# Kernel tuning notes

Hardware: AMD Instinct MI355X
Metric: run time of the kernel (lower is better)

The kernel has to match this reference:

```python
import jax, jax.numpy as jnp
import numpy as np

NUM_HEADS = 8
MAX_WS = 12


def _window_size(H, W, max_ws):
    common = [f for f in range(1, min(H, W) + 1) if H % f == 0 and W % f == 0 and f <= max_ws]
    return max(common) if common else min(H, W)


def _rel_index(ws):
    # static numpy computation, matches torch.meshgrid (ij) + offset logic
    coords = np.stack(np.meshgrid(np.arange(ws), np.arange(ws), indexing='ij')).reshape(2, -1)
    rel = coords[:, :, None] - coords[:, None, :]          # [2, ws^2, ws^2]
    rel = rel.transpose(1, 2, 0) + (ws - 1)                # [ws^2, ws^2, 2]
    return (rel[..., 0] * (2 * ws - 1) + rel[..., 1]).astype(np.int32)


def setup_inputs() -> dict:
    key = jax.random.key(0)
    ks = jax.random.split(key, 8)
    B, H, W, C = 8, 96, 96, 192
    N = H * W
    ws = _window_size(H, W, MAX_WS)  # 12
    x_seq = jax.random.normal(ks[0], (B, N, C), jnp.float32)
    noise_mask = jax.random.uniform(ks[1], (B, 1, H, W), jnp.float32)
    qkv_w = jax.random.normal(ks[2], (3 * C, C), jnp.float32) * 0.02
    qkv_b = jnp.zeros((3 * C,), jnp.float32)
    proj_w = jax.random.normal(ks[3], (C, C), jnp.float32) * 0.02
    proj_b = jnp.zeros((C,), jnp.float32)
    lpe_w = jax.random.normal(ks[4], (C, 1, 3, 3), jnp.float32) * 0.1  # depthwise OIHW
    lpe_b = jnp.zeros((C,), jnp.float32)
    lpe_scale = jnp.ones((1,), jnp.float32)
    bias_table = jax.random.normal(ks[5], ((2 * ws - 1) ** 2, NUM_HEADS), jnp.float32) * 0.02
    return {"x_seq": x_seq, "noise_mask": noise_mask, "qkv_w": qkv_w, "qkv_b": qkv_b,
            "proj_w": proj_w, "proj_b": proj_b, "lpe_w": lpe_w, "lpe_b": lpe_b,
            "lpe_scale": lpe_scale, "bias_table": bias_table}


def reference(x_seq, noise_mask, qkv_w, qkv_b, proj_w, proj_b, lpe_w, lpe_b, lpe_scale, bias_table):
    B, N, C = x_seq.shape
    H = W = int(round(N ** 0.5))
    heads = NUM_HEADS
    hd = C // heads
    ws = _window_size(H, W, MAX_WS)
    ws2 = ws * ws
    scale = hd ** (-0.5)

    x = x_seq.reshape(B, H, W, C)
    # window partition -> [nW, ws^2, C]
    win = x.reshape(B, H // ws, ws, W // ws, ws, C).transpose(0, 1, 3, 2, 4, 5).reshape(-1, ws2, C)

    qkv = win @ qkv_w.T + qkv_b                      # [nW, ws^2, 3C]
    qkv = qkv.reshape(-1, ws2, 3, heads, hd).transpose(2, 0, 3, 1, 4)  # [3, nW, h, ws^2, hd]
    q, k, v = qkv[0], qkv[1], qkv[2]

    attn = jnp.einsum('whqd,whkd->whqk', q, k) * scale   # [nW, h, ws^2, ws^2]
    idx = _rel_index(ws)                                  # static [ws^2, ws^2]
    bias = bias_table[idx.reshape(-1)].reshape(ws2, ws2, heads).transpose(2, 0, 1)
    attn = jax.nn.softmax(attn + bias[None], axis=-1)

    out = jnp.einsum('whqk,whkd->whqd', attn, v)          # [nW, h, ws^2, hd]
    out = out.transpose(0, 2, 1, 3).reshape(-1, ws2, C)
    out = out @ proj_w.T + proj_b

    # window reverse -> [B, H, W, C]
    x_attn = out.reshape(B, H // ws, W // ws, ws, ws, C).transpose(0, 1, 3, 2, 4, 5).reshape(B, H, W, C)

    # depthwise-conv LPE branch on NCHW input
    x_nchw = x.transpose(0, 3, 1, 2)
    lpe = jax.lax.conv_general_dilated(
        x_nchw, lpe_w, window_strides=(1, 1), padding='SAME',
        feature_group_count=C, dimension_numbers=('NCHW', 'OIHW', 'NCHW'))
    lpe = lpe + lpe_b[None, :, None, None]
    x_lpe = (lpe * lpe_scale[0] * noise_mask).transpose(0, 2, 3, 1)

    return (x_attn + x_lpe).reshape(B, N, C)
```

## Files before the change

### kernel.cpp

```cpp
#include <hip/hip_runtime.h>
#include <hip/hip_bf16.h>

constexpr int Bb   = 8;
constexpr int Hh   = 96;
constexpr int Ww   = 96;
constexpr int Cc   = 192;
constexpr int WS   = 12;
constexpr int WS2  = 144;
constexpr int HEADS= 8;
constexpr int HD   = 24;
constexpr int NWIN = Bb * (Hh/WS) * (Ww/WS);
constexpr int Mrows= NWIN * WS2;
constexpr int QKVN = 3 * Cc;

typedef __bf16 bf16x8 __attribute__((ext_vector_type(8)));
typedef float  f32x4  __attribute__((ext_vector_type(4)));

constexpr int LDP = 40;

__device__ __forceinline__ float us2f(unsigned short u) {
    unsigned int i = ((unsigned int)u) << 16;
    float f; __builtin_memcpy(&f, &i, 4);
    return f;
}
__device__ __forceinline__ unsigned short f2us(float f) {
    unsigned int i; __builtin_memcpy(&i, &f, 4);
    unsigned int lsb = (i >> 16) & 1u;
    i += 0x7fffu + lsb;
    return (unsigned short)(i >> 16);
}

__global__ __launch_bounds__(256) void qkv_gemm(
        const float* __restrict__ x,
        const float* __restrict__ w,
        const float* __restrict__ bias,
        unsigned short* __restrict__ qkv)
{
    __shared__ __bf16 As[128][LDP];
    __shared__ __bf16 Bs[64][LDP];

    const int tid = threadIdx.x;
    const int m0  = blockIdx.x * 128;
    const int n0  = blockIdx.y * 64;

    const int sa_row = tid >> 1;
    const int sa_ks  = (tid & 1) * 16;
    const int sb_row = tid >> 2;
    const int sb_ks  = (tid & 3) * 8;

    const int m    = m0 + sa_row;
    const int widx = m / WS2;
    const int pos  = m % WS2;
    const int b    = widx >> 6;
    const int wi   = (widx >> 3) & 7;
    const int wj   = widx & 7;
    const long xrow = ((long)((b * Hh + wi * WS + pos / WS) * Ww + wj * WS + pos % WS)) * Cc;
    const long brow = (long)(n0 + sb_row) * Cc;

    const int lane = tid & 63;
    const int wid  = tid >> 6;
    const int wm   = wid >> 1;
    const int wn   = wid & 1;
    const int frow = lane & 15;
    const int kblk = lane >> 4;

    f32x4 acc[4][2];
    #pragma unroll
    for (int i = 0; i < 4; ++i)
        #pragma unroll
        for (int j = 0; j < 2; ++j)
            acc[i][j] = f32x4{0.f, 0.f, 0.f, 0.f};

    for (int k0 = 0; k0 < Cc; k0 += 32) {
        {
            const float* g = x + xrow + k0 + sa_ks;
            float4 f0 = *reinterpret_cast<const float4*>(g);
            float4 f1 = *reinterpret_cast<const float4*>(g + 4);
            float4 f2 = *reinterpret_cast<const float4*>(g + 8);
            float4 f3 = *reinterpret_cast<const float4*>(g + 12);
            bf16x8 p0, p1;
            p0[0]=(__bf16)f0.x; p0[1]=(__bf16)f0.y; p0[2]=(__bf16)f0.z; p0[3]=(__bf16)f0.w;
            p0[4]=(__bf16)f1.x; p0[5]=(__bf16)f1.y; p0[6]=(__bf16)f1.z; p0[7]=(__bf16)f1.w;
            p1[0]=(__bf16)f2.x; p1[1]=(__bf16)f2.y; p1[2]=(__bf16)f2.z; p1[3]=(__bf16)f2.w;
            p1[4]=(__bf16)f3.x; p1[5]=(__bf16)f3.y; p1[6]=(__bf16)f3.z; p1[7]=(__bf16)f3.w;
            *reinterpret_cast<bf16x8*>(&As[sa_row][sa_ks])     = p0;
            *reinterpret_cast<bf16x8*>(&As[sa_row][sa_ks + 8]) = p1;
        }
        {
            const float* g = w + brow + k0 + sb_ks;
            float4 f0 = *reinterpret_cast<const float4*>(g);
            float4 f1 = *reinterpret_cast<const float4*>(g + 4);
            bf16x8 p0;
            p0[0]=(__bf16)f0.x; p0[1]=(__bf16)f0.y; p0[2]=(__bf16)f0.z; p0[3]=(__bf16)f0.w;
            p0[4]=(__bf16)f1.x; p0[5]=(__bf16)f1.y; p0[6]=(__bf16)f1.z; p0[7]=(__bf16)f1.w;
            *reinterpret_cast<bf16x8*>(&Bs[sb_row][sb_ks]) = p0;
        }
        __syncthreads();

        bf16x8 a0 = *reinterpret_cast<const bf16x8*>(&As[wm*64 +  0 + frow][kblk*8]);
        bf16x8 a1 = *reinterpret_cast<const bf16x8*>(&As[wm*64 + 16 + frow][kblk*8]);
        bf16x8 a2 = *reinterpret_cast<const bf16x8*>(&As[wm*64 + 32 + frow][kblk*8]);
        bf16x8 a3 = *reinterpret_cast<const bf16x8*>(&As[wm*64 + 48 + frow][kblk*8]);
        bf16x8 b0 = *reinterpret_cast<const bf16x8*>(&Bs[wn*32 +  0 + frow][kblk*8]);
        bf16x8 b1 = *reinterpret_cast<const bf16x8*>(&Bs[wn*32 + 16 + frow][kblk*8]);

        acc[0][0] = __builtin_amdgcn_mfma_f32_16x16x32_bf16(a0, b0, acc[0][0], 0, 0, 0);
        acc[0][1] = __builtin_amdgcn_mfma_f32_16x16x32_bf16(a0, b1, acc[0][1], 0, 0, 0);
        acc[1][0] = __builtin_amdgcn_mfma_f32_16x16x32_bf16(a1, b0, acc[1][0], 0, 0, 0);
        acc[1][1] = __builtin_amdgcn_mfma_f32_16x16x32_bf16(a1, b1, acc[1][1], 0, 0, 0);
        acc[2][0] = __builtin_amdgcn_mfma_f32_16x16x32_bf16(a2, b0, acc[2][0], 0, 0, 0);
        acc[2][1] = __builtin_amdgcn_mfma_f32_16x16x32_bf16(a2, b1, acc[2][1], 0, 0, 0);
        acc[3][0] = __builtin_amdgcn_mfma_f32_16x16x32_bf16(a3, b0, acc[3][0], 0, 0, 0);
        acc[3][1] = __builtin_amdgcn_mfma_f32_16x16x32_bf16(a3, b1, acc[3][1], 0, 0, 0);
        __syncthreads();
    }

    const int lrow = lane >> 4, lcol = lane & 15;
    #pragma unroll
    for (int fn = 0; fn < 2; ++fn) {
        const int c = n0 + wn*32 + fn*16 + lcol;
        const float bv = bias[c];
        #pragma unroll
        for (int fm = 0; fm < 4; ++fm) {
            const int rbase = m0 + wm*64 + fm*16 + lrow*4;
            #pragma unroll
            for (int r = 0; r < 4; ++r)
                qkv[(long)(rbase + r) * QKVN + c] = f2us(acc[fm][fn][r] + bv);
        }
    }
}

__global__ __launch_bounds__(192) void attn_kernel(
        const unsigned short* __restrict__ qkv,
        const float* __restrict__ btab,
        unsigned short* __restrict__ aout)
{
    __shared__ unsigned short Klds[WS2][40];
    __shared__ unsigned short Qlds[WS2][40];
    __shared__ unsigned short Vt[32][168];
    __shared__ unsigned short Pl[3][16][168];
    __shared__ float Bh[529];
    __shared__ unsigned short klut[WS2];
    __shared__ float l_inv[3][16];

    const int win  = blockIdx.x;
    const int head = blockIdx.y;
    const int tid  = threadIdx.x;

    const long base = (long)win * WS2 * QKVN;
    const int hoff  = head * HD;

    if (tid < WS2) {
        const uint4* qs = reinterpret_cast<const uint4*>(qkv + base + (long)tid * QKVN + hoff);
        const uint4* ks = reinterpret_cast<const uint4*>(qkv + base + (long)tid * QKVN + Cc + hoff);
        const uint4* vs = reinterpret_cast<const uint4*>(qkv + base + (long)tid * QKVN + 2*Cc + hoff);
        uint4 q0 = qs[0], q1 = qs[1], q2 = qs[2];
        uint4 k0 = ks[0], k1 = ks[1], k2 = ks[2];
        uint4 v0 = vs[0], v1 = vs[1], v2 = vs[2];
        *reinterpret_cast<uint4*>(&Qlds[tid][0])  = q0;
        *reinterpret_cast<uint4*>(&Qlds[tid][8])  = q1;
        *reinterpret_cast<uint4*>(&Qlds[tid][16]) = q2;
        *reinterpret_cast<uint4*>(&Qlds[tid][24]) = uint4{0,0,0,0};
        *reinterpret_cast<uint4*>(&Klds[tid][0])  = k0;
        *reinterpret_cast<uint4*>(&Klds[tid][8])  = k1;
        *reinterpret_cast<uint4*>(&Klds[tid][16]) = k2;
        *reinterpret_cast<uint4*>(&Klds[tid][24]) = uint4{0,0,0,0};
        unsigned short vr[24];
        __builtin_memcpy(&vr[0],  &v0, 16);
        __builtin_memcpy(&vr[8],  &v1, 16);
        __builtin_memcpy(&vr[16], &v2, 16);
        #pragma unroll
        for (int d = 0; d < HD; ++d)
            Vt[d][tid] = vr[d];
    }
    for (int e = tid; e < 8 * 160; e += 192)
        Vt[24 + e / 160][e % 160] = 0;
    for (int e = tid; e < 24 * 16; e += 192)
        Vt[e / 16][144 + (e & 15)] = 0;
    for (int e = tid; e < 529; e += 192)
        Bh[e] = btab[e * HEADS + head];
    if (tid < WS2)
        klut[tid] = (unsigned short)((tid / WS) * 23 + (tid % WS));
    __syncthreads();

    const int wv   = tid >> 6;
    const int lane = tid & 63;
    const int qcol = lane & 15;
    const int g    = lane >> 4;

    #pragma unroll
    for (int i = 0; i < 4; ++i) {
        const int e = lane + i * 64;
        Pl[wv][e >> 4][144 + (e & 15)] = 0;
    }

    const float scale = 0.2041241452319315f;

    #pragma unroll
    for (int ti = 0; ti < 3; ++ti) {
        const int qt = wv * 3 + ti;

        bf16x8 qb = *reinterpret_cast<const bf16x8*>(&Qlds[qt*16 + qcol][g*8]);
        f32x4 s[9];
        #pragma unroll
        for (int t = 0; t < 9; ++t) {
            bf16x8 ka = *reinterpret_cast<const bf16x8*>(&Klds[t*16 + qcol][g*8]);
            s[t] = __builtin_amdgcn_mfma_f32_16x16x32_bf16(ka, qb,
                     f32x4{0.f,0.f,0.f,0.f}, 0, 0, 0);
        }

        const int qpos = qt * 16 + qcol;
        const float bbase = (float)((qpos / WS + 11) * 23 + (qpos % WS + 11));
        float sv[9][4];
        float mx = -1e30f;
        #pragma unroll
        for (int t = 0; t < 9; ++t)
            #pragma unroll
            for (int r = 0; r < 4; ++r) {
                const int kv = t*16 + g*4 + r;
                const int rel = (int)bbase - (int)klut[kv];
                const float v = s[t][r] * scale + Bh[rel];
                sv[t][r] = v;
                mx = fmaxf(mx, v);
            }
        mx = fmaxf(mx, __shfl_xor(mx, 16));
        mx = fmaxf(mx, __shfl_xor(mx, 32));
        float sum = 0.f;
        #pragma unroll
        for (int t = 0; t < 9; ++t)
            #pragma unroll
            for (int r = 0; r < 4; ++r) {
                const float p = __expf(sv[t][r] - mx);
                sv[t][r] = p;
                sum += p;
            }
        sum += __shfl_xor(sum, 16);
        sum += __shfl_xor(sum, 32);
        if (g == 0)
            l_inv[wv][qcol] = 1.f / sum;

        #pragma unroll
        for (int t = 0; t < 9; ++t)
            #pragma unroll
            for (int r = 0; r < 4; ++r)
                Pl[wv][qcol][t*16 + g*4 + r] = f2us(sv[t][r]);

        f32x4 o0 = {0.f,0.f,0.f,0.f}, o1 = {0.f,0.f,0.f,0.f};
        #pragma unroll
        for (int ks = 0; ks < 5; ++ks) {
            bf16x8 pa  = *reinterpret_cast<const bf16x8*>(&Pl[wv][qcol][ks*32 + g*8]);
            bf16x8 vb0 = *reinterpret_cast<const bf16x8*>(&Vt[qcol     ][ks*32 + g*8]);
            bf16x8 vb1 = *reinterpret_cast<const bf16x8*>(&Vt[16 + qcol][ks*32 + g*8]);
            o0 = __builtin_amdgcn_mfma_f32_16x16x32_bf16(pa, vb0, o0, 0, 0, 0);
            o1 = __builtin_amdgcn_mfma_f32_16x16x32_bf16(pa, vb1, o1, 0, 0, 0);
        }

        #pragma unroll
        for (int idx = 0; idx < 4; ++idx) {
            const int qrow = qt*16 + g*4 + idx;
            const float li = l_inv[wv][g*4 + idx];
            const long ob = (long)(win * WS2 + qrow) * Cc + hoff;
            aout[ob + qcol] = f2us(o0[idx] * li);
            if (qcol < 8)
                aout[ob + 16 + qcol] = f2us(o1[idx] * li);
        }
    }
}

__global__ __launch_bounds__(256) void proj_gemm(
        const unsigned short* __restrict__ aout,
        const float* __restrict__ pw,
        const float* __restrict__ pb,
        float* __restrict__ out)
{
    __shared__ __bf16 As[128][LDP];
    __shared__ __bf16 Bs[64][LDP];

    const int tid = threadIdx.x;
    const int m0  = blockIdx.x * 128;
    const int n0  = blockIdx.y * 64;

    const int sa_row = tid >> 1;
    const int sa_ks  = (tid & 1) * 16;
    const int sb_row = tid >> 2;
    const int sb_ks  = (tid & 3) * 8;

    const long arow = (long)(m0 + sa_row) * Cc;
    const long brow = (long)(n0 + sb_row) * Cc;

    const int lane = tid & 63;
    const int wid  = tid >> 6;
    const int wm   = wid >> 1;
    const int wn   = wid & 1;
    const int frow = lane & 15;
    const int kblk = lane >> 4;

    f32x4 acc[4][2];
    #pragma unroll
    for (int i = 0; i < 4; ++i)
        #pragma unroll
        for (int j = 0; j < 2; ++j)
            acc[i][j] = f32x4{0.f, 0.f, 0.f, 0.f};

    for (int k0 = 0; k0 < Cc; k0 += 32) {
        {
            const unsigned short* g = aout + arow + k0 + sa_ks;
            uint4 v0 = *reinterpret_cast<const uint4*>(g);
            uint4 v1 = *reinterpret_cast<const uint4*>(g + 8);
            *reinterpret_cast<uint4*>(&As[sa_row][sa_ks])     = v0;
            *reinterpret_cast<uint4*>(&As[sa_row][sa_ks + 8]) = v1;
        }
        {
            const float* g = pw + brow + k0 + sb_ks;
            float4 f0 = *reinterpret_cast<const float4*>(g);
            float4 f1 = *reinterpret_cast<const float4*>(g + 4);
            bf16x8 p0;
            p0[0]=(__bf16)f0.x; p0[1]=(__bf16)f0.y; p0[2]=(__bf16)f0.z; p0[3]=(__bf16)f0.w;
            p0[4]=(__bf16)f1.x; p0[5]=(__bf16)f1.y; p0[6]=(__bf16)f1.z; p0[7]=(__bf16)f1.w;
            *reinterpret_cast<bf16x8*>(&Bs[sb_row][sb_ks]) = p0;
        }
        __syncthreads();

        bf16x8 a0 = *reinterpret_cast<const bf16x8*>(&As[wm*64 +  0 + frow][kblk*8]);
        bf16x8 a1 = *reinterpret_cast<const bf16x8*>(&As[wm*64 + 16 + frow][kblk*8]);
        bf16x8 a2 = *reinterpret_cast<const bf16x8*>(&As[wm*64 + 32 + frow][kblk*8]);
        bf16x8 a3 = *reinterpret_cast<const bf16x8*>(&As[wm*64 + 48 + frow][kblk*8]);
        bf16x8 b0 = *reinterpret_cast<const bf16x8*>(&Bs[wn*32 +  0 + frow][kblk*8]);
        bf16x8 b1 = *reinterpret_cast<const bf16x8*>(&Bs[wn*32 + 16 + frow][kblk*8]);

        acc[0][0] = __builtin_amdgcn_mfma_f32_16x16x32_bf16(a0, b0, acc[0][0], 0, 0, 0);
        acc[0][1] = __builtin_amdgcn_mfma_f32_16x16x32_bf16(a0, b1, acc[0][1], 0, 0, 0);
        acc[1][0] = __builtin_amdgcn_mfma_f32_16x16x32_bf16(a1, b0, acc[1][0], 0, 0, 0);
        acc[1][1] = __builtin_amdgcn_mfma_f32_16x16x32_bf16(a1, b1, acc[1][1], 0, 0, 0);
        acc[2][0] = __builtin_amdgcn_mfma_f32_16x16x32_bf16(a2, b0, acc[2][0], 0, 0, 0);
        acc[2][1] = __builtin_amdgcn_mfma_f32_16x16x32_bf16(a2, b1, acc[2][1], 0, 0, 0);
        acc[3][0] = __builtin_amdgcn_mfma_f32_16x16x32_bf16(a3, b0, acc[3][0], 0, 0, 0);
        acc[3][1] = __builtin_amdgcn_mfma_f32_16x16x32_bf16(a3, b1, acc[3][1], 0, 0, 0);
        __syncthreads();
    }

    const int lrow = lane >> 4, lcol = lane & 15;

    #pragma unroll
    for (int fm = 0; fm < 4; ++fm) {
        #pragma unroll
        for (int r = 0; r < 4; ++r) {
            const int mrow = m0 + wm*64 + fm*16 + lrow*4 + r;
            const int widx = mrow / WS2;
            const int pos  = mrow % WS2;
            const int b    = widx >> 6;
            const int wi   = (widx >> 3) & 7;
            const int wj   = widx & 7;
            const int h    = wi * WS + pos / WS;
            const int w_   = wj * WS + pos % WS;
            const long orow = ((long)(b * Hh + h) * Ww + w_) * Cc;

            #pragma unroll
            for (int fn = 0; fn < 2; ++fn) {
                const int c = n0 + wn*32 + fn*16 + lcol;
                out[orow + c] = acc[fm][fn][r] + pb[c];
            }
        }
    }
}

__global__ __launch_bounds__(256) void lpe_add(
        const float* __restrict__ x,
        const float* __restrict__ lw,
        const float* __restrict__ lb,
        const float* __restrict__ lsc,
        const float* __restrict__ mask,
        float* __restrict__ out)
{
    __shared__ float lwt[9][Cc];
    __shared__ float lbs[Cc];

    const int tid = threadIdx.x;
    for (int e = tid; e < Cc * 9; e += 256) {
        const int c = e / 9, tap = e % 9;
        lwt[tap][c] = lw[e];
    }
    for (int e = tid; e < Cc; e += 256)
        lbs[e] = lb[e];
    __syncthreads();

    const float ls = lsc[0];
    const long idx = (long)blockIdx.x * 256 + tid;
    const int c  = ((int)(idx % 48)) * 4;
    const int p  = (int)(idx / 48);
    const int w_ = p % Ww;
    const int h  = (p / Ww) % Hh;

    float4 acc = *reinterpret_cast<const float4*>(&lbs[c]);
    #pragma unroll
    for (int kh = -1; kh <= 1; ++kh) {
        const int hh = h + kh;
        if (hh < 0 || hh >= Hh) continue;
        #pragma unroll
        for (int kw = -1; kw <= 1; ++kw) {
            const int ww = w_ + kw;
            if (ww < 0 || ww >= Ww) continue;
            const float4 xv = *reinterpret_cast<const float4*>(
                x + ((long)p + kh * Ww + kw) * Cc + c);
            const float4 wv = *reinterpret_cast<const float4*>(&lwt[(kh+1)*3 + (kw+1)][c]);
            acc.x += xv.x * wv.x;
            acc.y += xv.y * wv.y;
            acc.z += xv.z * wv.z;
            acc.w += xv.w * wv.w;
        }
    }
    const float mv = mask[p] * ls;
    float* op = out + (long)p * Cc + c;
    float4 o = *reinterpret_cast<const float4*>(op);
    o.x += acc.x * mv;
    o.y += acc.y * mv;
    o.z += acc.z * mv;
    o.w += acc.w * mv;
    *reinterpret_cast<float4*>(op) = o;
}

extern "C" void kernel_launch(void* const* d_in, const int* in_sizes, int n_in,
                              void* d_out, int out_size, void* d_ws, size_t ws_size,
                              hipStream_t stream) {
    const float* x    = (const float*)d_in[0];
    const float* mask = (const float*)d_in[1];
    const float* qw   = (const float*)d_in[2];
    const float* qb   = (const float*)d_in[3];
    const float* pw   = (const float*)d_in[4];
    const float* pb   = (const float*)d_in[5];
    const float* lw   = (const float*)d_in[6];
    const float* lb   = (const float*)d_in[7];
    const float* lsc  = (const float*)d_in[8];
    const float* btab = (const float*)d_in[9];

    unsigned short* qkv  = (unsigned short*)d_ws;
    unsigned short* aout = qkv + (size_t)Mrows * QKVN;

    qkv_gemm<<<dim3(Mrows/128, QKVN/64), dim3(256), 0, stream>>>(x, qw, qb, qkv);
    attn_kernel<<<dim3(NWIN, HEADS), dim3(192), 0, stream>>>(qkv, btab, aout);
    proj_gemm<<<dim3(Mrows/128, Cc/64), dim3(256), 0, stream>>>(aout, pw, pb, (float*)d_out);
    lpe_add<<<dim3((Mrows * 48) / 256), dim3(256), 0, stream>>>(x, lw, lb, lsc, mask,
                                                                (float*)d_out);
}
```

Measured before the change: 340.5 us.

## Load Q/K directly into registers and reorder grids for L2 locality

```diff
diff --git a/kernel.cpp b/kernel.cpp
--- a/kernel.cpp
+++ b/kernel.cpp
@@ -16,7 +16,8 @@
 typedef __bf16 bf16x8 __attribute__((ext_vector_type(8)));
 typedef float  f32x4  __attribute__((ext_vector_type(4)));
 
-constexpr int LDP = 40;
+constexpr int LDP  = 40;
+constexpr int APAD = 170;
 
 __device__ __forceinline__ float us2f(unsigned short u) {
     unsigned int i = ((unsigned int)u) << 16;
@@ -40,8 +41,8 @@
     __shared__ __bf16 Bs[64][LDP];
 
     const int tid = threadIdx.x;
-    const int m0  = blockIdx.x * 128;
-    const int n0  = blockIdx.y * 64;
+    const int n0  = blockIdx.x * 64;
+    const int m0  = blockIdx.y * 128;
 
     const int sa_row = tid >> 1;
     const int sa_ks  = (tid & 1) * 16;
@@ -130,41 +131,27 @@
     }
 }
 
-__global__ __launch_bounds__(192) void attn_kernel(
+__global__ __launch_bounds__(192, 4) void attn_kernel(
         const unsigned short* __restrict__ qkv,
         const float* __restrict__ btab,
         unsigned short* __restrict__ aout)
 {
-    __shared__ unsigned short Klds[WS2][40];
-    __shared__ unsigned short Qlds[WS2][40];
-    __shared__ unsigned short Vt[32][168];
-    __shared__ unsigned short Pl[3][16][168];
+    __shared__ unsigned short Vt[32][APAD];
+    __shared__ unsigned short Pl[3][16][APAD];
     __shared__ float Bh[529];
     __shared__ unsigned short klut[WS2];
     __shared__ float l_inv[3][16];
 
-    const int win  = blockIdx.x;
-    const int head = blockIdx.y;
+    const int head = blockIdx.x;
+    const int win  = blockIdx.y;
     const int tid  = threadIdx.x;
 
     const long base = (long)win * WS2 * QKVN;
     const int hoff  = head * HD;
 
     if (tid < WS2) {
-        const uint4* qs = reinterpret_cast<const uint4*>(qkv + base + (long)tid * QKVN + hoff);
-        const uint4* ks = reinterpret_cast<const uint4*>(qkv + base + (long)tid * QKVN + Cc + hoff);
         const uint4* vs = reinterpret_cast<const uint4*>(qkv + base + (long)tid * QKVN + 2*Cc + hoff);
-        uint4 q0 = qs[0], q1 = qs[1], q2 = qs[2];
-        uint4 k0 = ks[0], k1 = ks[1], k2 = ks[2];
         uint4 v0 = vs[0], v1 = vs[1], v2 = vs[2];
-        *reinterpret_cast<uint4*>(&Qlds[tid][0])  = q0;
-        *reinterpret_cast<uint4*>(&Qlds[tid][8])  = q1;
-        *reinterpret_cast<uint4*>(&Qlds[tid][16]) = q2;
-        *reinterpret_cast<uint4*>(&Qlds[tid][24]) = uint4{0,0,0,0};
-        *reinterpret_cast<uint4*>(&Klds[tid][0])  = k0;
-        *reinterpret_cast<uint4*>(&Klds[tid][8])  = k1;
-        *reinterpret_cast<uint4*>(&Klds[tid][16]) = k2;
-        *reinterpret_cast<uint4*>(&Klds[tid][24]) = uint4{0,0,0,0};
         unsigned short vr[24];
         __builtin_memcpy(&vr[0],  &v0, 16);
         __builtin_memcpy(&vr[8],  &v1, 16);
@@ -181,18 +168,33 @@
         Bh[e] = btab[e * HEADS + head];
     if (tid < WS2)
         klut[tid] = (unsigned short)((tid / WS) * 23 + (tid % WS));
-    __syncthreads();
 
     const int wv   = tid >> 6;
     const int lane = tid & 63;
     const int qcol = lane & 15;
     const int g    = lane >> 4;
 
+    bf16x8 zerov;
+    #pragma unroll
+    for (int i = 0; i < 8; ++i) zerov[i] = (__bf16)0.0f;
+
+    bf16x8 ka[9];
+    if (g < 3) {
+        #pragma unroll
+        for (int t = 0; t < 9; ++t)
+            ka[t] = *reinterpret_cast<const bf16x8*>(
+                qkv + base + (long)(t*16 + qcol) * QKVN + Cc + hoff + g*8);
+    } else {
+        #pragma unroll
+        for (int t = 0; t < 9; ++t) ka[t] = zerov;
+    }
+
     #pragma unroll
     for (int i = 0; i < 4; ++i) {
         const int e = lane + i * 64;
         Pl[wv][e >> 4][144 + (e & 15)] = 0;
     }
+    __syncthreads();
 
     const float scale = 0.2041241452319315f;
 
@@ -200,14 +202,16 @@
     for (int ti = 0; ti < 3; ++ti) {
         const int qt = wv * 3 + ti;
 
-        bf16x8 qb = *reinterpret_cast<const bf16x8*>(&Qlds[qt*16 + qcol][g*8]);
+        bf16x8 qb = zerov;
+        if (g < 3)
+            qb = *reinterpret_cast<const bf16x8*>(
+                qkv + base + (long)(qt*16 + qcol) * QKVN + hoff + g*8);
+
         f32x4 s[9];
         #pragma unroll
-        for (int t = 0; t < 9; ++t) {
-            bf16x8 ka = *reinterpret_cast<const bf16x8*>(&Klds[t*16 + qcol][g*8]);
-            s[t] = __builtin_amdgcn_mfma_f32_16x16x32_bf16(ka, qb,
+        for (int t = 0; t < 9; ++t)
+            s[t] = __builtin_amdgcn_mfma_f32_16x16x32_bf16(ka[t], qb,
                      f32x4{0.f,0.f,0.f,0.f}, 0, 0, 0);
-        }
 
         const int qpos = qt * 16 + qcol;
         const float bbase = (float)((qpos / WS + 11) * 23 + (qpos % WS + 11));
@@ -277,8 +281,8 @@
     __shared__ __bf16 Bs[64][LDP];
 
     const int tid = threadIdx.x;
-    const int m0  = blockIdx.x * 128;
-    const int n0  = blockIdx.y * 64;
+    const int n0  = blockIdx.x * 64;
+    const int m0  = blockIdx.y * 128;
 
     const int sa_row = tid >> 1;
     const int sa_ks  = (tid & 1) * 16;
@@ -436,9 +440,9 @@
     unsigned short* qkv  = (unsigned short*)d_ws;
     unsigned short* aout = qkv + (size_t)Mrows * QKVN;
 
-    qkv_gemm<<<dim3(Mrows/128, QKVN/64), dim3(256), 0, stream>>>(x, qw, qb, qkv);
-    attn_kernel<<<dim3(NWIN, HEADS), dim3(192), 0, stream>>>(qkv, btab, aout);
-    proj_gemm<<<dim3(Mrows/128, Cc/64), dim3(256), 0, stream>>>(aout, pw, pb, (float*)d_out);
+    qkv_gemm<<<dim3(QKVN/64, Mrows/128), dim3(256), 0, stream>>>(x, qw, qb, qkv);
+    attn_kernel<<<dim3(HEADS, NWIN), dim3(192), 0, stream>>>(qkv, btab, aout);
+    proj_gemm<<<dim3(Cc/64, Mrows/128), dim3(256), 0, stream>>>(aout, pw, pb, (float*)d_out);
     lpe_add<<<dim3((Mrows * 48) / 256), dim3(256), 0, stream>>>(x, lw, lb, lsc, mask,
                                                                 (float*)d_out);
 }
```

Measured after the change: 336.8 us. No clear change (-1.1%).
